# Kernel optimization log

Measured on AMD Instinct MI355X. Metric: run time of the kernel, lower is better.

## Reference

```python
import jax, jax.numpy as jnp
import numpy as np

N_NODES = 50000
N_EDGES = 800000
D_IN, H1, H2, N_CLASSES = 128, 128, 64, 2


def setup_inputs() -> dict:
    key = jax.random.key(0)
    ks = jax.random.split(key, 8)
    x = jax.random.normal(ks[0], (N_NODES, D_IN), dtype=jnp.float32)
    edge_index = jax.random.randint(ks[1], (2, N_EDGES), 0, N_NODES, dtype=jnp.int64)
    s = 1.0 / np.sqrt(D_IN)
    W1 = jax.random.uniform(ks[2], (D_IN, H1), jnp.float32, -s, s)
    b1 = jnp.zeros((H1,), jnp.float32)
    s = 1.0 / np.sqrt(H1)
    W2 = jax.random.uniform(ks[3], (H1, H2), jnp.float32, -s, s)
    b2 = jnp.zeros((H2,), jnp.float32)
    s = 1.0 / np.sqrt(H2)
    Wo = jax.random.uniform(ks[4], (H2, N_CLASSES), jnp.float32, -s, s)
    bo = jax.random.uniform(ks[5], (N_CLASSES,), jnp.float32, -s, s)
    return {"x": x, "edge_index": edge_index, "W1": W1, "b1": b1,
            "W2": W2, "b2": b2, "Wo": Wo, "bo": bo}


def _gcn_conv(x, W, b, src, dst, n_nodes):
    # PyG GCNConv: add self loops, symmetric normalization deg^{-1/2} A deg^{-1/2}
    h = x @ W  # [N, out]
    ones = jnp.ones((src.shape[0],), h.dtype)
    deg = jax.ops.segment_sum(ones, dst, num_segments=n_nodes) + 1.0  # +1 self loop
    dinv = jax.lax.rsqrt(deg)  # deg >= 1 always (self loops)
    coef = dinv[src] * dinv[dst]  # [E]
    msg = h[src] * coef[:, None]  # [E, out] gather
    agg = jax.ops.segment_sum(msg, dst, num_segments=n_nodes)  # scatter-add
    agg = agg + h * (dinv * dinv)[:, None]  # self-loop contribution
    return agg + b


def reference(x, edge_index, W1, b1, W2, b2, Wo, bo):
    src, dst = edge_index[0], edge_index[1]
    n = x.shape[0]
    h = jax.nn.relu(_gcn_conv(x, W1, b1, src, dst, n))
    # dropout p=0.25 is identity in eval mode
    h = jax.nn.relu(_gcn_conv(h, W2, b2, src, dst, n))
    logits = h @ Wo + bo
    return jax.nn.log_softmax(logits, axis=1)
```

## Files before the change

### kernel.cpp

```cpp
#include <hip/hip_runtime.h>
#include <stdint.h>

#define N_NODES 50000
#define N_EDGES 800000
#define CAP 80
#define ZROW N_NODES
#define SCAT_BLOCKS 391
#define GEMM_BLOCKS 782

typedef __attribute__((ext_vector_type(8))) short short8;
typedef __attribute__((ext_vector_type(4))) float floatx4;

__device__ __forceinline__ float bflo(uint32_t u) { return __uint_as_float(u << 16); }
__device__ __forceinline__ float bfhi(uint32_t u) { return __uint_as_float(u & 0xffff0000u); }
__device__ __forceinline__ unsigned short f2b(float f) {
    uint32_t u = __float_as_uint(f);
    u += 0x7fffu + ((u >> 16) & 1u);
    return (unsigned short)(u >> 16);
}

__global__ void k_prep(const float* __restrict__ W1, const float* __restrict__ W2,
                       unsigned short* __restrict__ Wt1, unsigned short* __restrict__ Wt2,
                       int* __restrict__ counts) {
    int gid = blockIdx.x * 256 + threadIdx.x;
    if (gid < 16384) {
        int k = gid >> 7, n = gid & 127;
        Wt1[n * 128 + k] = f2b(W1[gid]);
    } else if (gid < 24576) {
        int j = gid - 16384;
        int k = j >> 6, n = j & 63;
        Wt2[n * 128 + k] = f2b(W2[j]);
    } else {
        counts[gid - 24576] = 0;
    }
}

__global__ __launch_bounds__(256) void k_scat_gemm1(const int* __restrict__ src,
                                                    const int* __restrict__ dst,
                                                    int* __restrict__ counts,
                                                    int* __restrict__ csr,
                                                    const float* __restrict__ x,
                                                    const unsigned short* __restrict__ Wt1,
                                                    unsigned short* __restrict__ h1s,
                                                    unsigned short* __restrict__ h2s) {
    __shared__ unsigned short At[64 * 136];
    __shared__ unsigned short Bt[128 * 136];
    int t = threadIdx.x;
    if (blockIdx.x < SCAT_BLOCKS) {
        int i = blockIdx.x * 256 + t;
        if (i >= N_EDGES / 8) return;
        const int4* s4 = (const int4*)(src + i * 8);
        const int4* d4 = (const int4*)(dst + i * 8);
        int4 sa = s4[0], sb = s4[1];
        int4 da = d4[0], db = d4[1];
        int r0 = atomicAdd(&counts[da.x], 1);
        int r1 = atomicAdd(&counts[da.y], 1);
        int r2 = atomicAdd(&counts[da.z], 1);
        int r3 = atomicAdd(&counts[da.w], 1);
        int r4 = atomicAdd(&counts[db.x], 1);
        int r5 = atomicAdd(&counts[db.y], 1);
        int r6 = atomicAdd(&counts[db.z], 1);
        int r7 = atomicAdd(&counts[db.w], 1);
        if (r0 < CAP) csr[da.x * CAP + r0] = sa.x;
        if (r1 < CAP) csr[da.y * CAP + r1] = sa.y;
        if (r2 < CAP) csr[da.z * CAP + r2] = sa.z;
        if (r3 < CAP) csr[da.w * CAP + r3] = sa.w;
        if (r4 < CAP) csr[db.x * CAP + r4] = sb.x;
        if (r5 < CAP) csr[db.y * CAP + r5] = sb.y;
        if (r6 < CAP) csr[db.z * CAP + r6] = sb.z;
        if (r7 < CAP) csr[db.w * CAP + r7] = sb.w;
        return;
    }
    int row0 = (blockIdx.x - SCAT_BLOCKS) * 64;
    for (int i = t; i < 2048; i += 256) {
        int n = i >> 4, kc = (i & 15) * 8;
        *(uint4*)&Bt[n * 136 + kc] = *(const uint4*)(Wt1 + n * 128 + kc);
    }
    for (int i = t; i < 1024; i += 256) {
        int r = i >> 4, kc = (i & 15) * 8;
        int g = row0 + r; if (g >= N_NODES) g = N_NODES - 1;
        const float* p = x + g * 128 + kc;
        float4 a = *(const float4*)p, b = *(const float4*)(p + 4);
        uint4 o;
        o.x = (uint32_t)f2b(a.x) | ((uint32_t)f2b(a.y) << 16);
        o.y = (uint32_t)f2b(a.z) | ((uint32_t)f2b(a.w) << 16);
        o.z = (uint32_t)f2b(b.x) | ((uint32_t)f2b(b.y) << 16);
        o.w = (uint32_t)f2b(b.z) | ((uint32_t)f2b(b.w) << 16);
        *(uint4*)&At[r * 136 + kc] = o;
    }
    __syncthreads();
    int wv = t >> 6, lane = t & 63;
    int m = lane & 15, qd = lane >> 4;
    floatx4 acc[8];
    #pragma unroll
    for (int c = 0; c < 8; c++) acc[c] = (floatx4){0.f, 0.f, 0.f, 0.f};
    const unsigned short* ap = &At[(wv * 16 + m) * 136 + qd * 8];
    const unsigned short* bp = &Bt[m * 136 + qd * 8];
    #pragma unroll
    for (int kk = 0; kk < 4; kk++) {
        short8 af = *(const short8*)(ap + kk * 32);
        #pragma unroll
        for (int c = 0; c < 8; c++) {
            short8 bf = *(const short8*)(bp + c * 16 * 136 + kk * 32);
            acc[c] = __builtin_amdgcn_mfma_f32_16x16x32_bf16(af, bf, acc[c], 0, 0, 0);
        }
    }
    #pragma unroll
    for (int reg = 0; reg < 4; reg++) {
        int g = row0 + wv * 16 + qd * 4 + reg;
        if (g < N_NODES) {
            #pragma unroll
            for (int c = 0; c < 8; c++)
                h1s[g * 128 + c * 16 + m] = f2b(acc[c][reg]);
        } else {
            #pragma unroll
            for (int c = 0; c < 8; c++)
                h1s[g * 128 + c * 16 + m] = 0;
            #pragma unroll
            for (int c = 0; c < 4; c++)
                h2s[g * 64 + c * 16 + m] = 0;
        }
    }
}

__global__ __launch_bounds__(256) void k_agg1g2(const unsigned short* __restrict__ h1s,
                                                const unsigned short* __restrict__ Wt2,
                                                const int* __restrict__ csr,
                                                const int* __restrict__ counts,
                                                const float* __restrict__ b1,
                                                unsigned short* __restrict__ h2s) {
    __shared__ unsigned short Bt[64 * 136];
    __shared__ unsigned short At[16 * 136];
    int t = threadIdx.x;
    for (int i = t; i < 1024; i += 256) {
        int n = i >> 4, kc = (i & 15) * 8;
        *(uint4*)&Bt[n * 136 + kc] = *(const uint4*)(Wt2 + n * 128 + kc);
    }
    int wv = t >> 6, lane = t & 63;
    int q = lane >> 4, l = lane & 15;
    int v0 = blockIdx.x * 16;
    int v = v0 + wv * 4 + q;
    int n = counts[v];
    float dv = rsqrtf((float)n + 1.0f);
    int n_eff = min(n, CAP);
    const int* cs = csr + v * CAP;
    int nmax = n_eff;
    nmax = max(nmax, __shfl_xor(nmax, 16));
    nmax = max(nmax, __shfl_xor(nmax, 32));
    float a0, a1, a2, a3, a4, a5, a6, a7;
    {
        uint4 p = *(const uint4*)(h1s + v * 128 + l * 8);
        a0 = dv * bflo(p.x); a1 = dv * bfhi(p.x); a2 = dv * bflo(p.y); a3 = dv * bfhi(p.y);
        a4 = dv * bflo(p.z); a5 = dv * bfhi(p.z); a6 = dv * bflo(p.w); a7 = dv * bfhi(p.w);
    }
    for (int base = 0; base < nmax; base += 16) {
        int idx = base + l;
        int e = (idx < n_eff) ? cs[idx] : ZROW;
        float de = rsqrtf((float)counts[e] + 1.0f);
        int mm = nmax - base; if (mm > 16) mm = 16;
        #pragma unroll 4
        for (int i = 0; i < mm; i++) {
            int s = __shfl(e, (q << 4) + i);
            float di = __shfl(de, (q << 4) + i);
            uint4 p = *(const uint4*)(h1s + s * 128 + l * 8);
            a0 = fmaf(di, bflo(p.x), a0); a1 = fmaf(di, bfhi(p.x), a1);
            a2 = fmaf(di, bflo(p.y), a2); a3 = fmaf(di, bfhi(p.y), a3);
            a4 = fmaf(di, bflo(p.z), a4); a5 = fmaf(di, bfhi(p.z), a5);
            a6 = fmaf(di, bflo(p.w), a6); a7 = fmaf(di, bfhi(p.w), a7);
        }
    }
    {
        float4 bL = *(const float4*)(b1 + l * 8);
        float4 bH = *(const float4*)(b1 + l * 8 + 4);
        a0 = fmaxf(fmaf(dv, a0, bL.x), 0.f); a1 = fmaxf(fmaf(dv, a1, bL.y), 0.f);
        a2 = fmaxf(fmaf(dv, a2, bL.z), 0.f); a3 = fmaxf(fmaf(dv, a3, bL.w), 0.f);
        a4 = fmaxf(fmaf(dv, a4, bH.x), 0.f); a5 = fmaxf(fmaf(dv, a5, bH.y), 0.f);
        a6 = fmaxf(fmaf(dv, a6, bH.z), 0.f); a7 = fmaxf(fmaf(dv, a7, bH.w), 0.f);
        uint4 o;
        o.x = (uint32_t)f2b(a0) | ((uint32_t)f2b(a1) << 16);
        o.y = (uint32_t)f2b(a2) | ((uint32_t)f2b(a3) << 16);
        o.z = (uint32_t)f2b(a4) | ((uint32_t)f2b(a5) << 16);
        o.w = (uint32_t)f2b(a6) | ((uint32_t)f2b(a7) << 16);
        *(uint4*)&At[(wv * 4 + q) * 136 + l * 8] = o;
    }
    __syncthreads();
    int m = lane & 15, qd = lane >> 4;
    floatx4 acc = (floatx4){0.f, 0.f, 0.f, 0.f};
    const unsigned short* ap = &At[m * 136 + qd * 8];
    const unsigned short* bp = &Bt[(wv * 16 + m) * 136 + qd * 8];
    #pragma unroll
    for (int kk = 0; kk < 4; kk++) {
        short8 af = *(const short8*)(ap + kk * 32);
        short8 bf = *(const short8*)(bp + kk * 32);
        acc = __builtin_amdgcn_mfma_f32_16x16x32_bf16(af, bf, acc, 0, 0, 0);
    }
    #pragma unroll
    for (int reg = 0; reg < 4; reg++) {
        int g = v0 + qd * 4 + reg;
        float dg = rsqrtf((float)counts[g] + 1.0f);
        h2s[g * 64 + wv * 16 + m] = f2b(dg * acc[reg]);
    }
}

__global__ __launch_bounds__(256) void k_agg2(const unsigned short* __restrict__ h2s,
                                              const int* __restrict__ csr,
                                              const int* __restrict__ counts,
                                              const float* __restrict__ b2,
                                              const float* __restrict__ Wo,
                                              const float* __restrict__ bo,
                                              float* __restrict__ out) {
    int wave = (blockIdx.x * 256 + threadIdx.x) >> 6;
    int lane = threadIdx.x & 63;
    int q = lane >> 4, l = lane & 15;
    int v = wave * 4 + q;
    int n = counts[v];
    float dv = rsqrtf((float)n + 1.0f);
    int n_eff = min(n, CAP);
    const int* cs = csr + v * CAP;
    int nmax = n_eff;
    nmax = max(nmax, __shfl_xor(nmax, 16));
    nmax = max(nmax, __shfl_xor(nmax, 32));
    float a0, a1, a2, a3;
    {
        uint2 p = *(const uint2*)(h2s + v * 64 + l * 4);
        a0 = bflo(p.x); a1 = bfhi(p.x); a2 = bflo(p.y); a3 = bfhi(p.y);
    }
    for (int base = 0; base < nmax; base += 16) {
        int idx = base + l;
        int e = (idx < n_eff) ? cs[idx] : ZROW;
        int mm = nmax - base; if (mm > 16) mm = 16;
        #pragma unroll 4
        for (int i = 0; i < mm; i++) {
            int s = __shfl(e, (q << 4) + i);
            uint2 p = *(const uint2*)(h2s + s * 64 + l * 4);
            a0 += bflo(p.x); a1 += bfhi(p.x); a2 += bflo(p.y); a3 += bfhi(p.y);
        }
    }
    float4 bb = *(const float4*)(b2 + l * 4);
    a0 = fmaxf(fmaf(dv, a0, bb.x), 0.f);
    a1 = fmaxf(fmaf(dv, a1, bb.y), 0.f);
    a2 = fmaxf(fmaf(dv, a2, bb.z), 0.f);
    a3 = fmaxf(fmaf(dv, a3, bb.w), 0.f);
    float4 w01 = *(const float4*)(Wo + l * 8);
    float4 w23 = *(const float4*)(Wo + l * 8 + 4);
    float l0 = a0 * w01.x + a1 * w01.z + a2 * w23.x + a3 * w23.z;
    float l1 = a0 * w01.y + a1 * w01.w + a2 * w23.y + a3 * w23.w;
    #pragma unroll
    for (int off = 8; off > 0; off >>= 1) {
        l0 += __shfl_xor(l0, off);
        l1 += __shfl_xor(l1, off);
    }
    if (l == 0) {
        float2 bof = *(const float2*)bo;
        l0 += bof.x; l1 += bof.y;
        float m = fmaxf(l0, l1);
        float ls = m + __logf(__expf(l0 - m) + __expf(l1 - m));
        *(float2*)(out + v * 2) = make_float2(l0 - ls, l1 - ls);
    }
}

extern "C" void kernel_launch(void* const* d_in, const int* in_sizes, int n_in,
                              void* d_out, int out_size, void* d_ws, size_t ws_size,
                              hipStream_t stream) {
    const float* x  = (const float*)d_in[0];
    const int* ei   = (const int*)d_in[1];
    const float* W1 = (const float*)d_in[2];
    const float* b1 = (const float*)d_in[3];
    const float* W2 = (const float*)d_in[4];
    const float* b2 = (const float*)d_in[5];
    const float* Wo = (const float*)d_in[6];
    const float* bo = (const float*)d_in[7];
    float* out      = (float*)d_out;
    const int* src = ei;
    const int* dst = ei + N_EDGES;

    char* w = (char*)d_ws;
    int* counts = (int*)(w + 0);
    int* csr    = (int*)(w + 200704);
    unsigned short* Wt1 = (unsigned short*)(w + 16200704);
    unsigned short* Wt2 = (unsigned short*)(w + 16233472);
    unsigned short* h1s = (unsigned short*)(w + 16249856);
    unsigned short* h2s = (unsigned short*)(w + 29062144);

    k_prep      <<<292, 256, 0, stream>>>(W1, W2, Wt1, Wt2, counts);
    k_scat_gemm1<<<SCAT_BLOCKS + GEMM_BLOCKS, 256, 0, stream>>>(src, dst, counts, csr,
                                                                x, Wt1, h1s, h2s);
    k_agg1g2    <<<3125, 256, 0, stream>>>(h1s, Wt2, csr, counts, b1, h2s);
    k_agg2      <<<3125, 256, 0, stream>>>(h2s, csr, counts, b2, Wo, bo, out);
}
```

Baseline: 186.8 us.

## Sort nodes by degree for load-balanced aggregation and split agg2 gather across half-lanes

Adds three small kernels that histogram node degrees, scan the bins and build a permutation that groups nodes of equal degree. Both aggregation kernels then process nodes in this order, so the four nodes sharing a wave have similar neighbour counts and fewer lanes sit idle in the per-wave max loop. Separately, k_agg2 now loads 16-byte rows with two half-groups handling alternate neighbours, then combines them with a shuffle. The cost is three extra launches plus a perm indirection, and output writes become scattered rather than contiguous.

```diff
diff --git a/kernel.cpp b/kernel.cpp
--- a/kernel.cpp
+++ b/kernel.cpp
@@ -5,6 +5,7 @@
 #define N_EDGES 800000
 #define CAP 80
 #define ZROW N_NODES
+#define NBIN 81
 #define SCAT_BLOCKS 391
 #define GEMM_BLOCKS 782
 
@@ -21,7 +22,7 @@
 
 __global__ void k_prep(const float* __restrict__ W1, const float* __restrict__ W2,
                        unsigned short* __restrict__ Wt1, unsigned short* __restrict__ Wt2,
-                       int* __restrict__ counts) {
+                       int* __restrict__ counts, int* __restrict__ bins) {
     int gid = blockIdx.x * 256 + threadIdx.x;
     if (gid < 16384) {
         int k = gid >> 7, n = gid & 127;
@@ -30,8 +31,10 @@
         int j = gid - 16384;
         int k = j >> 6, n = j & 63;
         Wt2[n * 128 + k] = f2b(W2[j]);
-    } else {
+    } else if (gid < 74752) {
         counts[gid - 24576] = 0;
+    } else if (gid < 74944) {
+        bins[gid - 74752] = 0;
     }
 }
 
@@ -123,10 +126,51 @@
     }
 }
 
+__global__ __launch_bounds__(256) void k_bin(const int* __restrict__ counts,
+                                             int* __restrict__ binCnt) {
+    __shared__ int lh[NBIN];
+    int t = threadIdx.x;
+    if (t < NBIN) lh[t] = 0;
+    __syncthreads();
+    int v = blockIdx.x * 256 + t;
+    if (v < N_NODES) atomicAdd(&lh[min(counts[v], CAP)], 1);
+    __syncthreads();
+    if (t < NBIN && lh[t] > 0) atomicAdd(&binCnt[t], lh[t]);
+}
+
+__global__ void k_scan(const int* __restrict__ binCnt, int* __restrict__ binOff) {
+    if (threadIdx.x == 0) {
+        int r = 0;
+        for (int i = 0; i < NBIN; i++) { binOff[i] = r; r += binCnt[i]; }
+    }
+}
+
+__global__ __launch_bounds__(256) void k_perm(const int* __restrict__ counts,
+                                              int* __restrict__ binOff,
+                                              int* __restrict__ perm) {
+    __shared__ int lh[NBIN];
+    __shared__ int lbase[NBIN];
+    int t = threadIdx.x;
+    if (t < NBIN) lh[t] = 0;
+    __syncthreads();
+    int v = blockIdx.x * 256 + t;
+    int d = 0, rank = 0;
+    bool act = (v < N_NODES);
+    if (act) {
+        d = min(counts[v], CAP);
+        rank = atomicAdd(&lh[d], 1);
+    }
+    __syncthreads();
+    if (t < NBIN && lh[t] > 0) lbase[t] = atomicAdd(&binOff[t], lh[t]);
+    __syncthreads();
+    if (act) perm[lbase[d] + rank] = v;
+}
+
 __global__ __launch_bounds__(256) void k_agg1g2(const unsigned short* __restrict__ h1s,
                                                 const unsigned short* __restrict__ Wt2,
                                                 const int* __restrict__ csr,
                                                 const int* __restrict__ counts,
+                                                const int* __restrict__ perm,
                                                 const float* __restrict__ b1,
                                                 unsigned short* __restrict__ h2s) {
     __shared__ unsigned short Bt[64 * 136];
@@ -139,7 +183,7 @@
     int wv = t >> 6, lane = t & 63;
     int q = lane >> 4, l = lane & 15;
     int v0 = blockIdx.x * 16;
-    int v = v0 + wv * 4 + q;
+    int v = perm[v0 + wv * 4 + q];
     int n = counts[v];
     float dv = rsqrtf((float)n + 1.0f);
     int n_eff = min(n, CAP);
@@ -196,15 +240,16 @@
     }
     #pragma unroll
     for (int reg = 0; reg < 4; reg++) {
-        int g = v0 + qd * 4 + reg;
-        float dg = rsqrtf((float)counts[g] + 1.0f);
-        h2s[g * 64 + wv * 16 + m] = f2b(dg * acc[reg]);
+        int pv = perm[v0 + qd * 4 + reg];
+        float dg = rsqrtf((float)counts[pv] + 1.0f);
+        h2s[pv * 64 + wv * 16 + m] = f2b(dg * acc[reg]);
     }
 }
 
 __global__ __launch_bounds__(256) void k_agg2(const unsigned short* __restrict__ h2s,
                                               const int* __restrict__ csr,
                                               const int* __restrict__ counts,
+                                              const int* __restrict__ perm,
                                               const float* __restrict__ b2,
                                               const float* __restrict__ Wo,
                                               const float* __restrict__ bo,
@@ -212,7 +257,8 @@
     int wave = (blockIdx.x * 256 + threadIdx.x) >> 6;
     int lane = threadIdx.x & 63;
     int q = lane >> 4, l = lane & 15;
-    int v = wave * 4 + q;
+    int h = l >> 3, c = l & 7;
+    int v = perm[wave * 4 + q];
     int n = counts[v];
     float dv = rsqrtf((float)n + 1.0f);
     int n_eff = min(n, CAP);
@@ -220,36 +266,46 @@
     int nmax = n_eff;
     nmax = max(nmax, __shfl_xor(nmax, 16));
     nmax = max(nmax, __shfl_xor(nmax, 32));
-    float a0, a1, a2, a3;
-    {
-        uint2 p = *(const uint2*)(h2s + v * 64 + l * 4);
+    float a0 = 0.f, a1 = 0.f, a2 = 0.f, a3 = 0.f, a4 = 0.f, a5 = 0.f, a6 = 0.f, a7 = 0.f;
+    if (h == 0) {
+        uint4 p = *(const uint4*)(h2s + v * 64 + c * 8);
         a0 = bflo(p.x); a1 = bfhi(p.x); a2 = bflo(p.y); a3 = bfhi(p.y);
+        a4 = bflo(p.z); a5 = bfhi(p.z); a6 = bflo(p.w); a7 = bfhi(p.w);
     }
     for (int base = 0; base < nmax; base += 16) {
         int idx = base + l;
         int e = (idx < n_eff) ? cs[idx] : ZROW;
         int mm = nmax - base; if (mm > 16) mm = 16;
+        int pairs = (mm + 1) >> 1;
         #pragma unroll 4
-        for (int i = 0; i < mm; i++) {
-            int s = __shfl(e, (q << 4) + i);
-            uint2 p = *(const uint2*)(h2s + s * 64 + l * 4);
+        for (int i = 0; i < pairs; i++) {
+            int s = __shfl(e, (q << 4) + 2 * i + h);
+            uint4 p = *(const uint4*)(h2s + s * 64 + c * 8);
             a0 += bflo(p.x); a1 += bfhi(p.x); a2 += bflo(p.y); a3 += bfhi(p.y);
+            a4 += bflo(p.z); a5 += bfhi(p.z); a6 += bflo(p.w); a7 += bfhi(p.w);
         }
     }
-    float4 bb = *(const float4*)(b2 + l * 4);
-    a0 = fmaxf(fmaf(dv, a0, bb.x), 0.f);
-    a1 = fmaxf(fmaf(dv, a1, bb.y), 0.f);
-    a2 = fmaxf(fmaf(dv, a2, bb.z), 0.f);
-    a3 = fmaxf(fmaf(dv, a3, bb.w), 0.f);
-    float4 w01 = *(const float4*)(Wo + l * 8);
-    float4 w23 = *(const float4*)(Wo + l * 8 + 4);
-    float l0 = a0 * w01.x + a1 * w01.z + a2 * w23.x + a3 * w23.z;
-    float l1 = a0 * w01.y + a1 * w01.w + a2 * w23.y + a3 * w23.w;
-    #pragma unroll
-    for (int off = 8; off > 0; off >>= 1) {
-        l0 += __shfl_xor(l0, off);
-        l1 += __shfl_xor(l1, off);
-    }
+    a0 += __shfl_xor(a0, 8); a1 += __shfl_xor(a1, 8);
+    a2 += __shfl_xor(a2, 8); a3 += __shfl_xor(a3, 8);
+    a4 += __shfl_xor(a4, 8); a5 += __shfl_xor(a5, 8);
+    a6 += __shfl_xor(a6, 8); a7 += __shfl_xor(a7, 8);
+    float4 bL = *(const float4*)(b2 + c * 8);
+    float4 bH = *(const float4*)(b2 + c * 8 + 4);
+    a0 = fmaxf(fmaf(dv, a0, bL.x), 0.f); a1 = fmaxf(fmaf(dv, a1, bL.y), 0.f);
+    a2 = fmaxf(fmaf(dv, a2, bL.z), 0.f); a3 = fmaxf(fmaf(dv, a3, bL.w), 0.f);
+    a4 = fmaxf(fmaf(dv, a4, bH.x), 0.f); a5 = fmaxf(fmaf(dv, a5, bH.y), 0.f);
+    a6 = fmaxf(fmaf(dv, a6, bH.z), 0.f); a7 = fmaxf(fmaf(dv, a7, bH.w), 0.f);
+    float4 wA = *(const float4*)(Wo + c * 16);
+    float4 wB = *(const float4*)(Wo + c * 16 + 4);
+    float4 wC = *(const float4*)(Wo + c * 16 + 8);
+    float4 wD = *(const float4*)(Wo + c * 16 + 12);
+    float l0 = a0 * wA.x + a1 * wA.z + a2 * wB.x + a3 * wB.z
+             + a4 * wC.x + a5 * wC.z + a6 * wD.x + a7 * wD.z;
+    float l1 = a0 * wA.y + a1 * wA.w + a2 * wB.y + a3 * wB.w
+             + a4 * wC.y + a5 * wC.w + a6 * wD.y + a7 * wD.w;
+    l0 += __shfl_xor(l0, 1); l1 += __shfl_xor(l1, 1);
+    l0 += __shfl_xor(l0, 2); l1 += __shfl_xor(l1, 2);
+    l0 += __shfl_xor(l0, 4); l1 += __shfl_xor(l1, 4);
     if (l == 0) {
         float2 bof = *(const float2*)bo;
         l0 += bof.x; l1 += bof.y;
@@ -281,10 +337,17 @@
     unsigned short* Wt2 = (unsigned short*)(w + 16233472);
     unsigned short* h1s = (unsigned short*)(w + 16249856);
     unsigned short* h2s = (unsigned short*)(w + 29062144);
-
-    k_prep      <<<292, 256, 0, stream>>>(W1, W2, Wt1, Wt2, counts);
+    int* perm   = (int*)(w + 35468288);
+    int* bins   = (int*)(w + 35668288);
+    int* binCnt = bins;
+    int* binOff = bins + 96;
+
+    k_prep      <<<293, 256, 0, stream>>>(W1, W2, Wt1, Wt2, counts, bins);
     k_scat_gemm1<<<SCAT_BLOCKS + GEMM_BLOCKS, 256, 0, stream>>>(src, dst, counts, csr,
                                                                 x, Wt1, h1s, h2s);
-    k_agg1g2    <<<3125, 256, 0, stream>>>(h1s, Wt2, csr, counts, b1, h2s);
-    k_agg2      <<<3125, 256, 0, stream>>>(h2s, csr, counts, b2, Wo, bo, out);
-}
+    k_bin       <<<196, 256, 0, stream>>>(counts, binCnt);
+    k_scan      <<<1, 64, 0, stream>>>(binCnt, binOff);
+    k_perm      <<<196, 256, 0, stream>>>(counts, binOff, perm);
+    k_agg1g2    <<<3125, 256, 0, stream>>>(h1s, Wt2, csr, counts, perm, b1, h2s);
+    k_agg2      <<<3125, 256, 0, stream>>>(h2s, csr, counts, perm, b2, Wo, bo, out);
+}
```

Measured after the change: 195.0 us. 1.04x slower.

## Pad degree counters to 64B stride and widen layer-2 gather to 16B loads

Applied to the files above, without the earlier changes.

Each node's degree counter now sits at a 16-int (64-byte) stride, so atomics to different nodes no longer share a cache line and contend with each other. The zeroing pass and the workspace layout grow to cover the padded array. The layer-2 aggregation kernel now has each half of a 16-lane group take alternate neighbors with 16-byte loads, then combines the two halves with a shuffle. This raises bytes per load, at the cost of a larger counts footprint and scattered degree reads in the aggregation kernels.

```diff
diff --git a/kernel.cpp b/kernel.cpp
--- a/kernel.cpp
+++ b/kernel.cpp
@@ -7,6 +7,7 @@
 #define ZROW N_NODES
 #define SCAT_BLOCKS 391
 #define GEMM_BLOCKS 782
+#define CNT(v) ((v) << 4)
 
 typedef __attribute__((ext_vector_type(8))) short short8;
 typedef __attribute__((ext_vector_type(4))) float floatx4;
@@ -30,7 +31,7 @@
         int j = gid - 16384;
         int k = j >> 6, n = j & 63;
         Wt2[n * 128 + k] = f2b(W2[j]);
-    } else {
+    } else if (gid < 24576 + 802816) {
         counts[gid - 24576] = 0;
     }
 }
@@ -53,14 +54,14 @@
         const int4* d4 = (const int4*)(dst + i * 8);
         int4 sa = s4[0], sb = s4[1];
         int4 da = d4[0], db = d4[1];
-        int r0 = atomicAdd(&counts[da.x], 1);
-        int r1 = atomicAdd(&counts[da.y], 1);
-        int r2 = atomicAdd(&counts[da.z], 1);
-        int r3 = atomicAdd(&counts[da.w], 1);
-        int r4 = atomicAdd(&counts[db.x], 1);
-        int r5 = atomicAdd(&counts[db.y], 1);
-        int r6 = atomicAdd(&counts[db.z], 1);
-        int r7 = atomicAdd(&counts[db.w], 1);
+        int r0 = atomicAdd(&counts[CNT(da.x)], 1);
+        int r1 = atomicAdd(&counts[CNT(da.y)], 1);
+        int r2 = atomicAdd(&counts[CNT(da.z)], 1);
+        int r3 = atomicAdd(&counts[CNT(da.w)], 1);
+        int r4 = atomicAdd(&counts[CNT(db.x)], 1);
+        int r5 = atomicAdd(&counts[CNT(db.y)], 1);
+        int r6 = atomicAdd(&counts[CNT(db.z)], 1);
+        int r7 = atomicAdd(&counts[CNT(db.w)], 1);
         if (r0 < CAP) csr[da.x * CAP + r0] = sa.x;
         if (r1 < CAP) csr[da.y * CAP + r1] = sa.y;
         if (r2 < CAP) csr[da.z * CAP + r2] = sa.z;
@@ -140,7 +141,7 @@
     int q = lane >> 4, l = lane & 15;
     int v0 = blockIdx.x * 16;
     int v = v0 + wv * 4 + q;
-    int n = counts[v];
+    int n = counts[CNT(v)];
     float dv = rsqrtf((float)n + 1.0f);
     int n_eff = min(n, CAP);
     const int* cs = csr + v * CAP;
@@ -156,7 +157,7 @@
     for (int base = 0; base < nmax; base += 16) {
         int idx = base + l;
         int e = (idx < n_eff) ? cs[idx] : ZROW;
-        float de = rsqrtf((float)counts[e] + 1.0f);
+        float de = rsqrtf((float)counts[CNT(e)] + 1.0f);
         int mm = nmax - base; if (mm > 16) mm = 16;
         #pragma unroll 4
         for (int i = 0; i < mm; i++) {
@@ -197,7 +198,7 @@
     #pragma unroll
     for (int reg = 0; reg < 4; reg++) {
         int g = v0 + qd * 4 + reg;
-        float dg = rsqrtf((float)counts[g] + 1.0f);
+        float dg = rsqrtf((float)counts[CNT(g)] + 1.0f);
         h2s[g * 64 + wv * 16 + m] = f2b(dg * acc[reg]);
     }
 }
@@ -212,44 +213,55 @@
     int wave = (blockIdx.x * 256 + threadIdx.x) >> 6;
     int lane = threadIdx.x & 63;
     int q = lane >> 4, l = lane & 15;
+    int h = l >> 3, c = l & 7;
     int v = wave * 4 + q;
-    int n = counts[v];
+    int n = counts[CNT(v)];
     float dv = rsqrtf((float)n + 1.0f);
     int n_eff = min(n, CAP);
     const int* cs = csr + v * CAP;
     int nmax = n_eff;
     nmax = max(nmax, __shfl_xor(nmax, 16));
     nmax = max(nmax, __shfl_xor(nmax, 32));
-    float a0, a1, a2, a3;
-    {
-        uint2 p = *(const uint2*)(h2s + v * 64 + l * 4);
+    float a0 = 0.f, a1 = 0.f, a2 = 0.f, a3 = 0.f, a4 = 0.f, a5 = 0.f, a6 = 0.f, a7 = 0.f;
+    if (h == 0) {
+        uint4 p = *(const uint4*)(h2s + v * 64 + c * 8);
         a0 = bflo(p.x); a1 = bfhi(p.x); a2 = bflo(p.y); a3 = bfhi(p.y);
+        a4 = bflo(p.z); a5 = bfhi(p.z); a6 = bflo(p.w); a7 = bfhi(p.w);
     }
     for (int base = 0; base < nmax; base += 16) {
         int idx = base + l;
         int e = (idx < n_eff) ? cs[idx] : ZROW;
         int mm = nmax - base; if (mm > 16) mm = 16;
+        int pairs = (mm + 1) >> 1;
         #pragma unroll 4
-        for (int i = 0; i < mm; i++) {
-            int s = __shfl(e, (q << 4) + i);
-            uint2 p = *(const uint2*)(h2s + s * 64 + l * 4);
+        for (int i = 0; i < pairs; i++) {
+            int s = __shfl(e, (q << 4) + 2 * i + h);
+            uint4 p = *(const uint4*)(h2s + s * 64 + c * 8);
             a0 += bflo(p.x); a1 += bfhi(p.x); a2 += bflo(p.y); a3 += bfhi(p.y);
+            a4 += bflo(p.z); a5 += bfhi(p.z); a6 += bflo(p.w); a7 += bfhi(p.w);
         }
     }
-    float4 bb = *(const float4*)(b2 + l * 4);
-    a0 = fmaxf(fmaf(dv, a0, bb.x), 0.f);
-    a1 = fmaxf(fmaf(dv, a1, bb.y), 0.f);
-    a2 = fmaxf(fmaf(dv, a2, bb.z), 0.f);
-    a3 = fmaxf(fmaf(dv, a3, bb.w), 0.f);
-    float4 w01 = *(const float4*)(Wo + l * 8);
-    float4 w23 = *(const float4*)(Wo + l * 8 + 4);
-    float l0 = a0 * w01.x + a1 * w01.z + a2 * w23.x + a3 * w23.z;
-    float l1 = a0 * w01.y + a1 * w01.w + a2 * w23.y + a3 * w23.w;
-    #pragma unroll
-    for (int off = 8; off > 0; off >>= 1) {
-        l0 += __shfl_xor(l0, off);
-        l1 += __shfl_xor(l1, off);
-    }
+    a0 += __shfl_xor(a0, 8); a1 += __shfl_xor(a1, 8);
+    a2 += __shfl_xor(a2, 8); a3 += __shfl_xor(a3, 8);
+    a4 += __shfl_xor(a4, 8); a5 += __shfl_xor(a5, 8);
+    a6 += __shfl_xor(a6, 8); a7 += __shfl_xor(a7, 8);
+    float4 bL = *(const float4*)(b2 + c * 8);
+    float4 bH = *(const float4*)(b2 + c * 8 + 4);
+    a0 = fmaxf(fmaf(dv, a0, bL.x), 0.f); a1 = fmaxf(fmaf(dv, a1, bL.y), 0.f);
+    a2 = fmaxf(fmaf(dv, a2, bL.z), 0.f); a3 = fmaxf(fmaf(dv, a3, bL.w), 0.f);
+    a4 = fmaxf(fmaf(dv, a4, bH.x), 0.f); a5 = fmaxf(fmaf(dv, a5, bH.y), 0.f);
+    a6 = fmaxf(fmaf(dv, a6, bH.z), 0.f); a7 = fmaxf(fmaf(dv, a7, bH.w), 0.f);
+    float4 wA = *(const float4*)(Wo + c * 16);
+    float4 wB = *(const float4*)(Wo + c * 16 + 4);
+    float4 wC = *(const float4*)(Wo + c * 16 + 8);
+    float4 wD = *(const float4*)(Wo + c * 16 + 12);
+    float l0 = a0 * wA.x + a1 * wA.z + a2 * wB.x + a3 * wB.z
+             + a4 * wC.x + a5 * wC.z + a6 * wD.x + a7 * wD.z;
+    float l1 = a0 * wA.y + a1 * wA.w + a2 * wB.y + a3 * wB.w
+             + a4 * wC.y + a5 * wC.w + a6 * wD.y + a7 * wD.w;
+    l0 += __shfl_xor(l0, 1); l1 += __shfl_xor(l1, 1);
+    l0 += __shfl_xor(l0, 2); l1 += __shfl_xor(l1, 2);
+    l0 += __shfl_xor(l0, 4); l1 += __shfl_xor(l1, 4);
     if (l == 0) {
         float2 bof = *(const float2*)bo;
         l0 += bof.x; l1 += bof.y;
@@ -276,13 +288,13 @@
 
     char* w = (char*)d_ws;
     int* counts = (int*)(w + 0);
-    int* csr    = (int*)(w + 200704);
-    unsigned short* Wt1 = (unsigned short*)(w + 16200704);
-    unsigned short* Wt2 = (unsigned short*)(w + 16233472);
-    unsigned short* h1s = (unsigned short*)(w + 16249856);
-    unsigned short* h2s = (unsigned short*)(w + 29062144);
-
-    k_prep      <<<292, 256, 0, stream>>>(W1, W2, Wt1, Wt2, counts);
+    int* csr    = (int*)(w + 3211264);
+    unsigned short* Wt1 = (unsigned short*)(w + 19211264);
+    unsigned short* Wt2 = (unsigned short*)(w + 19244032);
+    unsigned short* h1s = (unsigned short*)(w + 19260416);
+    unsigned short* h2s = (unsigned short*)(w + 32072704);
+
+    k_prep      <<<3232, 256, 0, stream>>>(W1, W2, Wt1, Wt2, counts);
     k_scat_gemm1<<<SCAT_BLOCKS + GEMM_BLOCKS, 256, 0, stream>>>(src, dst, counts, csr,
                                                                 x, Wt1, h1s, h2s);
     k_agg1g2    <<<3125, 256, 0, stream>>>(h1s, Wt2, csr, counts, b1, h2s);
```

Result: no change. 183.9 us (-1.6%).
